# Kernel tuning notes

Hardware: AMD Instinct MI355X
Metric: run time of the kernel (lower is better)

Reference implementation:

```python
import jax, jax.numpy as jnp
import numpy as np

VOCAB = 4194304
EMBED = 128
BATCH = 16384
NUM_DENSE = 13
NUM_CAT = 26
BOT_DIMS = (512, 256, 128)
TOP_DIMS = (1024, 1024, 512, 256, 1)


def _dense_params(key, fan_in, fan_out):
    kw, kb = jax.random.split(key)
    w = jax.random.normal(kw, (fan_in, fan_out), jnp.float32) * np.sqrt(2.0 / (fan_in + fan_out))
    b = jax.random.normal(kb, (fan_out,), jnp.float32) * np.sqrt(1.0 / fan_out)
    return w, b


def setup_inputs() -> dict:
    key = jax.random.key(0)
    ks = jax.random.split(key, 16)
    inp = {}
    inp['x_dense'] = jax.random.normal(ks[0], (BATCH, NUM_DENSE), jnp.float32)
    inp['x_cat'] = jax.random.randint(ks[1], (BATCH, NUM_CAT), 0, VOCAB, dtype=jnp.int32)
    # embedding table: uniform(0,1) * 1/sqrt(vocab)
    inp['embedding_table'] = jax.random.uniform(ks[2], (VOCAB, EMBED), jnp.float32) * np.float32(1.0 / np.sqrt(VOCAB))
    # bottom MLP params
    fan_in = NUM_DENSE
    for i, d in enumerate(BOT_DIMS):
        w, b = _dense_params(ks[3 + i], fan_in, d)
        inp[f'w_bot{i}'], inp[f'b_bot{i}'] = w, b
        fan_in = d
    # top MLP params; input dim = embed_dim + n_triu(27) = 128 + 378 = 506
    n_feat = 1 + NUM_CAT  # 27
    fan_in = EMBED + n_feat * (n_feat + 1) // 2
    for i, d in enumerate(TOP_DIMS):
        w, b = _dense_params(ks[8 + i], fan_in, d)
        inp[f'w_top{i}'], inp[f'b_top{i}'] = w, b
        fan_in = d
    return inp


def _forward(x_dense, x_cat, embedding_table,
             w_bot0, b_bot0, w_bot1, b_bot1, w_bot2, b_bot2,
             w_top0, b_top0, w_top1, b_top1, w_top2, b_top2,
             w_top3, b_top3, w_top4, b_top4):
    B = x_dense.shape[0]
    # bottom MLP
    h = x_dense
    for w, b in ((w_bot0, b_bot0), (w_bot1, b_bot1), (w_bot2, b_bot2)):
        h = jax.nn.relu(h @ w + b)
    bot_out = h  # [B, 128]
    feat = bot_out.reshape(B, -1, EMBED)  # [B, 1, 128]
    # embedding gather (irregular access)
    idx = (x_cat.reshape(-1) % VOCAB)
    emb = embedding_table[idx].reshape(B, NUM_CAT, EMBED)  # [B, 26, 128]
    stack = jnp.concatenate([feat, emb], axis=1)  # [B, 27, 128]
    # self interaction + upper-triangular (incl. diagonal) extraction
    xact = jnp.einsum('bnd,bmd->bnm', stack, stack)  # [B, 27, 27]
    i, j = jnp.triu_indices(stack.shape[1])
    inter = xact[:, i, j]  # [B, 378]
    top = jnp.concatenate([bot_out, inter], axis=-1)  # [B, 506]
    tops = ((w_top0, b_top0), (w_top1, b_top1), (w_top2, b_top2), (w_top3, b_top3), (w_top4, b_top4))
    for li, (w, b) in enumerate(tops):
        top = top @ w + b
        if li < len(tops) - 1:
            top = jax.nn.relu(top)
    return top  # [B, 1] logits


def reference(x_dense, x_cat, embedding_table,
              w_bot0, b_bot0, w_bot1, b_bot1, w_bot2, b_bot2,
              w_top0, b_top0, w_top1, b_top1, w_top2, b_top2,
              w_top3, b_top3, w_top4, b_top4):
    return _forward(x_dense, x_cat, embedding_table,
                    w_bot0, b_bot0, w_bot1, b_bot1, w_bot2, b_bot2,
                    w_top0, b_top0, w_top1, b_top1, w_top2, b_top2,
                    w_top3, b_top3, w_top4, b_top4)
```

## Files before the change

### kernel.cpp

```cpp
#include <hip/hip_runtime.h>
#include <cstdint>
#include <cstddef>

#define BATCH 16384
#define VOCAB_MASK (4194304 - 1)

typedef __attribute__((ext_vector_type(4))) float f32x4;
typedef __attribute__((ext_vector_type(8))) __bf16 bf16x8;

static_assert(sizeof(bf16x8) == 16, "bf16x8 must be 16 bytes");

static __device__ __forceinline__ __bf16 f2bf(float f) {
  union { float f; unsigned u; } in; in.f = f;
  unsigned r = in.u + 0x7FFF + ((in.u >> 16) & 1);
  union { unsigned short s; __bf16 b; } out; out.s = (unsigned short)(r >> 16);
  return out.b;
}
static __device__ __forceinline__ float bf2f(__bf16 b) {
  union { __bf16 b; unsigned short s; } in; in.b = b;
  union { unsigned u; float f; } out; out.u = ((unsigned)in.s) << 16;
  return out.f;
}

#define GLDS16(g, l) __builtin_amdgcn_global_load_lds( \
    (const __attribute__((address_space(1))) unsigned int*)(g), \
    (__attribute__((address_space(3))) unsigned int*)(l), 16, 0, 0)

static __device__ __forceinline__ unsigned swz16(unsigned b) {
  return b ^ ((((b >> 6) & 3u) ^ ((b >> 8) & 3u)) << 4);
}
static __device__ __forceinline__ bf16x8 lds_frag(const char* smem, unsigned base,
                                                  unsigned r, unsigned cg) {
  unsigned b = r * 64u + cg;
  return *(const bf16x8*)(smem + base + swz16(b));
}

struct TJob { const float* W; __bf16* WT; int K, N, Kp, tx, off; };
struct TJobs { TJob j[7]; };

__global__ __launch_bounds__(256) void transpose_all(TJobs js, int njobs)
{
  __shared__ float tile[64][65];
  int b = blockIdx.x;
  int ji = 0;
  #pragma unroll
  for (int i = 1; i < 7; ++i) if (i < njobs && b >= js.j[i].off) ji = i;
  const TJob jb = js.j[ji];
  int lb = b - jb.off;
  int bx = lb % jb.tx, by = lb / jb.tx;
  const int kb = bx * 64, nb = by * 64;
  const int tx = threadIdx.x & 63, ty = threadIdx.x >> 6;
  #pragma unroll
  for (int i = 0; i < 64; i += 4) {
    int k = kb + ty + i, n = nb + tx;
    tile[ty + i][tx] = (k < jb.K && n < jb.N) ? jb.W[(size_t)k * jb.N + n] : 0.f;
  }
  __syncthreads();
  #pragma unroll
  for (int i = 0; i < 64; i += 4) {
    int n = nb + ty + i, k = kb + tx;
    if (n < jb.N && k < jb.Kp) jb.WT[(size_t)n * jb.Kp + k] = f2bf(tile[tx][ty + i]);
  }
}

__global__ __launch_bounds__(512, 2) void gemm_8ph(
    const __bf16* __restrict__ A, const __bf16* __restrict__ WT,
    const float* __restrict__ bias, __bf16* __restrict__ C,
    int N, int sA, int K, int gm)
{
  __shared__ __align__(16) char smem[65536];
  const int tid = threadIdx.x, lane = tid & 63, w = tid >> 6;
  const int wm = w >> 2, wn = w & 3;

  int nb = gridDim.x;
  int id = blockIdx.x;
  int swz = ((nb & 7) == 0) ? ((id & 7) * (nb >> 3) + (id >> 3)) : id;
  const int m0 = (swz % gm) * 256, n0 = (swz / gm) * 256;

  unsigned Ld[2]; const __bf16* sAp[2]; const __bf16* sBp[2];
  #pragma unroll
  for (int h = 0; h < 2; ++h) {
    unsigned L = h * 8192u + (unsigned)w * 1024u + (unsigned)lane * 16u;
    unsigned Ls = swz16(L);
    Ld[h] = L;
    int srow = Ls >> 6, scb = Ls & 63;
    sAp[h] = A  + (size_t)(m0 + srow) * sA + (scb >> 1);
    sBp[h] = WT + (size_t)(n0 + srow) * K  + (scb >> 1);
  }

  #define STAGE_A(kt, p) { GLDS16(sAp[0] + (kt)*32, smem + (p)*32768 + Ld[0]); \
                           GLDS16(sAp[1] + (kt)*32, smem + (p)*32768 + Ld[1]); }
  #define STAGE_B(kt, p) { GLDS16(sBp[0] + (kt)*32, smem + (p)*32768 + 16384 + Ld[0]); \
                           GLDS16(sBp[1] + (kt)*32, smem + (p)*32768 + 16384 + Ld[1]); }

  const unsigned cg = (lane >> 4) * 16u;
  const unsigned rA = (lane & 15);

  f32x4 acc[8][4] = {};
  const int KT = K >> 5;
  const int iters = KT >> 1;

  STAGE_B(0, 0); STAGE_A(0, 0); STAGE_B(1, 1);
  asm volatile("s_waitcnt vmcnt(2)" ::: "memory");
  __builtin_amdgcn_s_barrier();
  __builtin_amdgcn_sched_barrier(0);

  for (int i = 0; i < iters; ++i) {
    const int t = 2 * i;
    const bool more = (i + 1 < iters);

    bf16x8 a0[4], b0[4];
    #pragma unroll
    for (int m = 0; m < 4; ++m) a0[m] = lds_frag(smem, 0, wm * 128 + m * 16 + rA, cg);
    #pragma unroll
    for (int n = 0; n < 4; ++n) b0[n] = lds_frag(smem, 16384, wn * 64 + n * 16 + rA, cg);
    STAGE_A(t + 1, 1);
    __builtin_amdgcn_s_barrier();
    asm volatile("s_waitcnt lgkmcnt(0)" ::: "memory");
    __builtin_amdgcn_sched_barrier(0);
    __builtin_amdgcn_s_setprio(1);
    #pragma unroll
    for (int m = 0; m < 4; ++m)
      #pragma unroll
      for (int n = 0; n < 4; ++n)
        acc[m][n] = __builtin_amdgcn_mfma_f32_16x16x32_bf16(a0[m], b0[n], acc[m][n], 0, 0, 0);
    __builtin_amdgcn_s_setprio(0);
    __builtin_amdgcn_s_barrier();
    __builtin_amdgcn_sched_barrier(0);

    bf16x8 a1[4];
    #pragma unroll
    for (int m = 0; m < 4; ++m) a1[m] = lds_frag(smem, 0, wm * 128 + 64 + m * 16 + rA, cg);
    if (more) STAGE_B(t + 2, 0);
    __builtin_amdgcn_s_barrier();
    asm volatile("s_waitcnt lgkmcnt(0)" ::: "memory");
    __builtin_amdgcn_sched_barrier(0);
    __builtin_amdgcn_s_setprio(1);
    #pragma unroll
    for (int m = 0; m < 4; ++m)
      #pragma unroll
      for (int n = 0; n < 4; ++n)
        acc[4 + m][n] = __builtin_amdgcn_mfma_f32_16x16x32_bf16(a1[m], b0[n], acc[4 + m][n], 0, 0, 0);
    __builtin_amdgcn_s_setprio(0);
    if (more) { asm volatile("s_waitcnt vmcnt(2)" ::: "memory"); }
    else      { asm volatile("s_waitcnt vmcnt(0)" ::: "memory"); }
    __builtin_amdgcn_s_barrier();
    __builtin_amdgcn_sched_barrier(0);

    bf16x8 a2[4], b2[4];
    #pragma unroll
    for (int m = 0; m < 4; ++m) a2[m] = lds_frag(smem, 32768, wm * 128 + m * 16 + rA, cg);
    #pragma unroll
    for (int n = 0; n < 4; ++n) b2[n] = lds_frag(smem, 32768 + 16384, wn * 64 + n * 16 + rA, cg);
    if (more) STAGE_A(t + 2, 0);
    __builtin_amdgcn_s_barrier();
    asm volatile("s_waitcnt lgkmcnt(0)" ::: "memory");
    __builtin_amdgcn_sched_barrier(0);
    __builtin_amdgcn_s_setprio(1);
    #pragma unroll
    for (int m = 0; m < 4; ++m)
      #pragma unroll
      for (int n = 0; n < 4; ++n)
        acc[m][n] = __builtin_amdgcn_mfma_f32_16x16x32_bf16(a2[m], b2[n], acc[m][n], 0, 0, 0);
    __builtin_amdgcn_s_setprio(0);
    __builtin_amdgcn_s_barrier();
    __builtin_amdgcn_sched_barrier(0);

    bf16x8 a3[4];
    #pragma unroll
    for (int m = 0; m < 4; ++m) a3[m] = lds_frag(smem, 32768, wm * 128 + 64 + m * 16 + rA, cg);
    if (more) STAGE_B(t + 3, 1);
    __builtin_amdgcn_s_barrier();
    asm volatile("s_waitcnt lgkmcnt(0)" ::: "memory");
    __builtin_amdgcn_sched_barrier(0);
    __builtin_amdgcn_s_setprio(1);
    #pragma unroll
    for (int m = 0; m < 4; ++m)
      #pragma unroll
      for (int n = 0; n < 4; ++n)
        acc[4 + m][n] = __builtin_amdgcn_mfma_f32_16x16x32_bf16(a3[m], b2[n], acc[4 + m][n], 0, 0, 0);
    __builtin_amdgcn_s_setprio(0);
    if (more) { asm volatile("s_waitcnt vmcnt(2)" ::: "memory"); }
    __builtin_amdgcn_s_barrier();
    __builtin_amdgcn_sched_barrier(0);
  }

  #pragma unroll
  for (int n = 0; n < 4; ++n) {
    int col = n0 + wn * 64 + n * 16 + (lane & 15);
    float bv = bias[col];
    #pragma unroll
    for (int m = 0; m < 8; ++m) {
      #pragma unroll
      for (int r = 0; r < 4; ++r) {
        int row = m0 + wm * 128 + m * 16 + (lane >> 4) * 4 + r;
        float v = fmaxf(acc[m][n][r] + bv, 0.f);
        C[(size_t)row * N + col] = f2bf(v);
      }
    }
  }
  #undef STAGE_A
  #undef STAGE_B
}

__global__ __launch_bounds__(256) void gemm_glds(
    const __bf16* __restrict__ A, const __bf16* __restrict__ WT,
    const float* __restrict__ bias, __bf16* __restrict__ C,
    int N, int sA, int Kp)
{
  __shared__ __bf16 As[128][32];
  __shared__ __bf16 Bs[128][32];
  const int tid  = threadIdx.x;
  const int lane = tid & 63;
  const int wid  = tid >> 6;
  const int wr = wid >> 1, wc = wid & 1;
  const int m0 = blockIdx.x * 128, n0 = blockIdx.y * 128;

  const int srow = wid * 16 + (lane >> 2);
  const int scol = (lane & 3) * 8;
  const __bf16* Ag0 = A  + (size_t)(m0 + srow)      * sA + scol;
  const __bf16* Ag1 = A  + (size_t)(m0 + srow + 64) * sA + scol;
  const __bf16* Bg0 = WT + (size_t)(n0 + srow)      * Kp + scol;
  const __bf16* Bg1 = WT + (size_t)(n0 + srow + 64) * Kp + scol;
  __bf16* lA0 = &As[srow][scol];
  __bf16* lA1 = &As[srow + 64][scol];
  __bf16* lB0 = &Bs[srow][scol];
  __bf16* lB1 = &Bs[srow + 64][scol];

  f32x4 acc[4][4] = {};

  for (int k0 = 0; k0 < Kp; k0 += 32) {
    __syncthreads();
    GLDS16(Ag0 + k0, lA0);
    GLDS16(Ag1 + k0, lA1);
    GLDS16(Bg0 + k0, lB0);
    GLDS16(Bg1 + k0, lB1);
    __syncthreads();

    bf16x8 af[4], bfv[4];
    #pragma unroll
    for (int m = 0; m < 4; ++m)
      af[m] = *(const bf16x8*)&As[wr * 64 + m * 16 + (lane & 15)][(lane >> 4) * 8];
    #pragma unroll
    for (int n = 0; n < 4; ++n)
      bfv[n] = *(const bf16x8*)&Bs[wc * 64 + n * 16 + (lane & 15)][(lane >> 4) * 8];
    #pragma unroll
    for (int m = 0; m < 4; ++m)
      #pragma unroll
      for (int n = 0; n < 4; ++n)
        acc[m][n] = __builtin_amdgcn_mfma_f32_16x16x32_bf16(af[m], bfv[n], acc[m][n], 0, 0, 0);
  }

  #pragma unroll
  for (int m = 0; m < 4; ++m)
    #pragma unroll
    for (int n = 0; n < 4; ++n) {
      int col = n0 + wc * 64 + n * 16 + (lane & 15);
      float bv = bias[col];
      #pragma unroll
      for (int r = 0; r < 4; ++r) {
        int row = m0 + wr * 64 + m * 16 + (lane >> 4) * 4 + r;
        float v = fmaxf(acc[m][n][r] + bv, 0.f);
        C[(size_t)row * N + col] = f2bf(v);
      }
    }
}

__global__ __launch_bounds__(256) void gemm_f32a(
    const float* __restrict__ A, const __bf16* __restrict__ WT,
    const float* __restrict__ bias, __bf16* __restrict__ C,
    int N, int sA, int Kb, int Kp)
{
  __shared__ __bf16 As[128][40];
  __shared__ __bf16 Bs[128][40];
  const int tid  = threadIdx.x;
  const int lane = tid & 63;
  const int wid  = tid >> 6;
  const int wr = wid >> 1, wc = wid & 1;
  const int m0 = blockIdx.x * 128, n0 = blockIdx.y * 128;
  const int lrow = tid >> 2;
  const int lkk  = (tid & 3) * 8;

  f32x4 acc[4][4] = {};

  for (int k0 = 0; k0 < Kp; k0 += 32) {
    __syncthreads();
    #pragma unroll
    for (int it = 0; it < 2; ++it) {
      int row = lrow + it * 64;
      #pragma unroll
      for (int j = 0; j < 8; ++j) {
        int k = k0 + lkk + j;
        float v = (k < Kb) ? A[(size_t)(m0 + row) * sA + k] : 0.f;
        As[row][lkk + j] = f2bf(v);
      }
      *(bf16x8*)&Bs[row][lkk] = *(const bf16x8*)&WT[(size_t)(n0 + row) * Kp + k0 + lkk];
    }
    __syncthreads();

    bf16x8 af[4], bfv[4];
    #pragma unroll
    for (int m = 0; m < 4; ++m)
      af[m] = *(const bf16x8*)&As[wr * 64 + m * 16 + (lane & 15)][(lane >> 4) * 8];
    #pragma unroll
    for (int n = 0; n < 4; ++n)
      bfv[n] = *(const bf16x8*)&Bs[wc * 64 + n * 16 + (lane & 15)][(lane >> 4) * 8];
    #pragma unroll
    for (int m = 0; m < 4; ++m)
      #pragma unroll
      for (int n = 0; n < 4; ++n)
        acc[m][n] = __builtin_amdgcn_mfma_f32_16x16x32_bf16(af[m], bfv[n], acc[m][n], 0, 0, 0);
  }

  #pragma unroll
  for (int m = 0; m < 4; ++m)
    #pragma unroll
    for (int n = 0; n < 4; ++n) {
      int col = n0 + wc * 64 + n * 16 + (lane & 15);
      float bv = bias[col];
      #pragma unroll
      for (int r = 0; r < 4; ++r) {
        int row = m0 + wr * 64 + m * 16 + (lane >> 4) * 4 + r;
        float v = fmaxf(acc[m][n][r] + bv, 0.f);
        C[(size_t)row * N + col] = f2bf(v);
      }
    }
}

__global__ __launch_bounds__(256) void interact_mfma(
    const __bf16* __restrict__ bot, const int* __restrict__ xcat,
    const float* __restrict__ emb, __bf16* __restrict__ top_in)
{
  __shared__ __bf16 st[4][32][136];
  const int tid = threadIdx.x, lane = tid & 63, w = tid >> 6;
  const int s = blockIdx.x * 4 + w;

  {
    const __bf16* bp = bot + (size_t)s * 128 + lane * 2;
    st[w][0][lane * 2]     = bp[0];
    st[w][0][lane * 2 + 1] = bp[1];
  }
  const int* xr = xcat + (size_t)s * 26;
  #pragma unroll
  for (int r = 1; r < 27; ++r) {
    int ridx = xr[r - 1] & VOCAB_MASK;
    float2 v = *(const float2*)(emb + (size_t)ridx * 128 + lane * 2);
    st[w][r][lane * 2]     = f2bf(v.x);
    st[w][r][lane * 2 + 1] = f2bf(v.y);
  }
  #pragma unroll
  for (int r = 27; r < 32; ++r) {
    st[w][r][lane * 2]     = f2bf(0.f);
    st[w][r][lane * 2 + 1] = f2bf(0.f);
  }

  f32x4 a00 = {}, a01 = {}, a11 = {};
  #pragma unroll
  for (int k0 = 0; k0 < 4; ++k0) {
    bf16x8 fr0 = *(const bf16x8*)&st[w][(lane & 15)][k0 * 32 + (lane >> 4) * 8];
    bf16x8 fr1 = *(const bf16x8*)&st[w][16 + (lane & 15)][k0 * 32 + (lane >> 4) * 8];
    a00 = __builtin_amdgcn_mfma_f32_16x16x32_bf16(fr0, fr0, a00, 0, 0, 0);
    a01 = __builtin_amdgcn_mfma_f32_16x16x32_bf16(fr0, fr1, a01, 0, 0, 0);
    a11 = __builtin_amdgcn_mfma_f32_16x16x32_bf16(fr1, fr1, a11, 0, 0, 0);
  }

  __bf16* op = top_in + (size_t)s * 512;
  op[lane * 2]     = st[w][0][lane * 2];
  op[lane * 2 + 1] = st[w][0][lane * 2 + 1];
  if (lane < 6) op[506 + lane] = f2bf(0.f);

  const int jc = lane & 15, rb = (lane >> 4) * 4;
  #pragma unroll
  for (int r = 0; r < 4; ++r) {
    {
      int i = rb + r, j = jc;
      if (i <= j) op[128 + i * 27 - i * (i - 1) / 2 + (j - i)] = f2bf(a00[r]);
    }
    {
      int i = rb + r, j = 16 + jc;
      if (j <= 26) op[128 + i * 27 - i * (i - 1) / 2 + (j - i)] = f2bf(a01[r]);
    }
    {
      int i = 16 + rb + r, j = 16 + jc;
      if (i <= j && j <= 26) op[128 + i * 27 - i * (i - 1) / 2 + (j - i)] = f2bf(a11[r]);
    }
  }
}

__global__ __launch_bounds__(256) void final_kernel(
    const __bf16* __restrict__ t3, const float* __restrict__ w4,
    const float* __restrict__ b4, float* __restrict__ out)
{
  int row  = blockIdx.x * 4 + (threadIdx.x >> 6);
  int lane = threadIdx.x & 63;
  const __bf16* tr = &t3[(size_t)row * 256 + lane * 4];
  float acc = 0.f;
  #pragma unroll
  for (int j = 0; j < 4; ++j) acc += bf2f(tr[j]) * w4[lane * 4 + j];
  #pragma unroll
  for (int off = 32; off; off >>= 1) acc += __shfl_down(acc, off);
  if (lane == 0) out[row] = acc + b4[0];
}

extern "C" void kernel_launch(void* const* d_in, const int* in_sizes, int n_in,
                              void* d_out, int out_size, void* d_ws, size_t ws_size,
                              hipStream_t stream)
{
  const float* x_dense = (const float*)d_in[0];
  const int*   x_cat   = (const int*)d_in[1];
  const float* emb     = (const float*)d_in[2];
  const float* wb[3] = {(const float*)d_in[3], (const float*)d_in[5], (const float*)d_in[7]};
  const float* bb[3] = {(const float*)d_in[4], (const float*)d_in[6], (const float*)d_in[8]};
  const float* wt[5] = {(const float*)d_in[9],  (const float*)d_in[11], (const float*)d_in[13],
                        (const float*)d_in[15], (const float*)d_in[17]};
  const float* bt[5] = {(const float*)d_in[10], (const float*)d_in[12], (const float*)d_in[14],
                        (const float*)d_in[16], (const float*)d_in[18]};
  float* out = (float*)d_out;

  char* ws = (char*)d_ws;
  const size_t MB = 1ull << 20;
  __bf16* wt_b0 = (__bf16*)(ws + 0 * MB);
  __bf16* wt_b1 = (__bf16*)(ws + 1 * MB);
  __bf16* wt_b2 = (__bf16*)(ws + 2 * MB);
  __bf16* wt_t0 = (__bf16*)(ws + 3 * MB);
  __bf16* wt_t1 = (__bf16*)(ws + 4 * MB);
  __bf16* wt_t2 = (__bf16*)(ws + 6 * MB);
  __bf16* wt_t3 = (__bf16*)(ws + 7 * MB);
  __bf16* h2     = (__bf16*)(ws + 8 * MB);
  __bf16* top_in = (__bf16*)(ws + 12 * MB);
  __bf16* t2     = (__bf16*)(ws + 12 * MB);
  __bf16* h0     = (__bf16*)(ws + 28 * MB);
  __bf16* t1     = (__bf16*)(ws + 28 * MB);
  __bf16* t3     = (__bf16*)(ws + 28 * MB);
  __bf16* h1     = (__bf16*)(ws + 60 * MB);
  __bf16* t0     = (__bf16*)(ws + 60 * MB);

  TJobs js;
  const float* Ws[7] = {wb[0], wb[1], wb[2], wt[0], wt[1], wt[2], wt[3]};
  __bf16* WTs[7] = {wt_b0, wt_b1, wt_b2, wt_t0, wt_t1, wt_t2, wt_t3};
  int Ks[7]  = {13, 512, 256, 506, 1024, 1024, 512};
  int Ns[7]  = {512, 256, 128, 1024, 1024, 512, 256};
  int Kps[7] = {32, 512, 256, 512, 1024, 1024, 512};
  int off = 0;
  for (int i = 0; i < 7; ++i) {
    int tx = (Kps[i] + 63) / 64, ty = (Ns[i] + 63) / 64;
    js.j[i] = TJob{Ws[i], WTs[i], Ks[i], Ns[i], Kps[i], tx, off};
    off += tx * ty;
  }
  transpose_all<<<dim3(off), dim3(256), 0, stream>>>(js, 7);

  gemm_f32a<<<dim3(128, 4), dim3(256), 0, stream>>>(x_dense, wt_b0, bb[0], h0, 512, 13, 13, 32);
  gemm_glds<<<dim3(128, 2), dim3(256), 0, stream>>>(h0, wt_b1, bb[1], h1, 256, 512, 512);
  gemm_glds<<<dim3(128, 1), dim3(256), 0, stream>>>(h1, wt_b2, bb[2], h2, 128, 256, 256);

  interact_mfma<<<dim3(BATCH / 4), dim3(256), 0, stream>>>(h2, x_cat, emb, top_in);

  gemm_8ph<<<dim3(256), dim3(512), 0, stream>>>(top_in, wt_t0, bt[0], t0, 1024, 512, 512, 64);
  gemm_8ph<<<dim3(256), dim3(512), 0, stream>>>(t0, wt_t1, bt[1], t1, 1024, 1024, 1024, 64);
  gemm_glds<<<dim3(128, 4), dim3(256), 0, stream>>>(t1, wt_t2, bt[2], t2, 512, 1024, 1024);
  gemm_glds<<<dim3(128, 2), dim3(256), 0, stream>>>(t2, wt_t3, bt[3], t3, 256, 512, 512);

  final_kernel<<<dim3(BATCH / 4), dim3(256), 0, stream>>>(t3, wt[4], bt[4], out);
}
```

Baseline: 214.6 us.

## Fuse bottom MLP into one kernel and use pipelined 256x128 GEMM for top layer 2

The three bottom-MLP GEMM launches are merged into one kernel. Each 32-row block computes h0 and h1 in shared memory and writes only h2, which removes two launches and the global round trips of the h0/h1 intermediates. The third top-MLP layer (N=512) moves from the simple gemm_glds kernel to a new software-pipelined 256x128 tile variant of gemm_8ph, for better MFMA utilisation. The fused bottom kernel uses small 32-row tiles and reloads weight tiles in every block, which may limit its efficiency.

```diff
diff --git a/kernel.cpp b/kernel.cpp
--- a/kernel.cpp
+++ b/kernel.cpp
@@ -61,6 +61,130 @@
     int n = nb + ty + i, k = kb + tx;
     if (n < jb.N && k < jb.Kp) jb.WT[(size_t)n * jb.Kp + k] = f2bf(tile[tx][ty + i]);
   }
+}
+
+__global__ __launch_bounds__(256) void bottom_fused(
+    const float* __restrict__ x,
+    const __bf16* __restrict__ w0t, const float* __restrict__ b0,
+    const __bf16* __restrict__ w1t, const float* __restrict__ b1,
+    const __bf16* __restrict__ w2t, const float* __restrict__ b2,
+    __bf16* __restrict__ h2out)
+{
+  __shared__ __bf16 h0s[32][520];
+  __shared__ __bf16 h1s[32][264];
+  __shared__ __bf16 As[32][40];
+  __shared__ __bf16 Bs[256][32];
+  const int tid = threadIdx.x, lane = tid & 63, w = tid >> 6;
+  const int r0 = blockIdx.x * 32;
+  const int srow_b = lane >> 2;
+  const int scol_b = (lane & 3) * 8;
+  const unsigned rA = lane & 15, cgw = (lane >> 4) * 8;
+
+  for (int idx = tid; idx < 32 * 40; idx += 256) {
+    int row = idx / 40, k = idx - row * 40;
+    float v = (k < 13) ? x[(size_t)(r0 + row) * 13 + k] : 0.f;
+    As[row][k] = f2bf(v);
+  }
+
+  #pragma unroll
+  for (int p = 0; p < 2; ++p) {
+    __syncthreads();
+    #pragma unroll
+    for (int c = 0; c < 4; ++c) {
+      int row = w * 64 + c * 16 + srow_b;
+      GLDS16(w0t + (size_t)(p * 256 + row) * 32 + scol_b, &Bs[row][scol_b]);
+    }
+    __syncthreads();
+    bf16x8 a[2], bv[4];
+    #pragma unroll
+    for (int m = 0; m < 2; ++m) a[m] = *(const bf16x8*)&As[rA + m * 16][cgw];
+    #pragma unroll
+    for (int n = 0; n < 4; ++n) bv[n] = *(const bf16x8*)&Bs[w * 64 + n * 16 + rA][cgw];
+    f32x4 acc[2][4] = {};
+    #pragma unroll
+    for (int m = 0; m < 2; ++m)
+      #pragma unroll
+      for (int n = 0; n < 4; ++n)
+        acc[m][n] = __builtin_amdgcn_mfma_f32_16x16x32_bf16(a[m], bv[n], acc[m][n], 0, 0, 0);
+    #pragma unroll
+    for (int m = 0; m < 2; ++m)
+      #pragma unroll
+      for (int n = 0; n < 4; ++n) {
+        int col = p * 256 + w * 64 + n * 16 + (int)rA;
+        float bb = b0[col];
+        #pragma unroll
+        for (int r = 0; r < 4; ++r) {
+          int row = m * 16 + (lane >> 4) * 4 + r;
+          h0s[row][col] = f2bf(fmaxf(acc[m][n][r] + bb, 0.f));
+        }
+      }
+  }
+
+  f32x4 acc1[2][4] = {};
+  for (int k0 = 0; k0 < 512; k0 += 32) {
+    __syncthreads();
+    #pragma unroll
+    for (int c = 0; c < 4; ++c) {
+      int row = w * 64 + c * 16 + srow_b;
+      GLDS16(w1t + (size_t)row * 512 + k0 + scol_b, &Bs[row][scol_b]);
+    }
+    __syncthreads();
+    bf16x8 a[2], bv[4];
+    #pragma unroll
+    for (int m = 0; m < 2; ++m) a[m] = *(const bf16x8*)&h0s[rA + m * 16][k0 + cgw];
+    #pragma unroll
+    for (int n = 0; n < 4; ++n) bv[n] = *(const bf16x8*)&Bs[w * 64 + n * 16 + rA][cgw];
+    #pragma unroll
+    for (int m = 0; m < 2; ++m)
+      #pragma unroll
+      for (int n = 0; n < 4; ++n)
+        acc1[m][n] = __builtin_amdgcn_mfma_f32_16x16x32_bf16(a[m], bv[n], acc1[m][n], 0, 0, 0);
+  }
+  #pragma unroll
+  for (int m = 0; m < 2; ++m)
+    #pragma unroll
+    for (int n = 0; n < 4; ++n) {
+      int col = w * 64 + n * 16 + (int)rA;
+      float bb = b1[col];
+      #pragma unroll
+      for (int r = 0; r < 4; ++r) {
+        int row = m * 16 + (lane >> 4) * 4 + r;
+        h1s[row][col] = f2bf(fmaxf(acc1[m][n][r] + bb, 0.f));
+      }
+    }
+
+  f32x4 acc2[2][2] = {};
+  for (int k0 = 0; k0 < 256; k0 += 32) {
+    __syncthreads();
+    #pragma unroll
+    for (int c = 0; c < 2; ++c) {
+      int row = w * 32 + c * 16 + srow_b;
+      GLDS16(w2t + (size_t)row * 256 + k0 + scol_b, &Bs[row][scol_b]);
+    }
+    __syncthreads();
+    bf16x8 a[2], bv[2];
+    #pragma unroll
+    for (int m = 0; m < 2; ++m) a[m] = *(const bf16x8*)&h1s[rA + m * 16][k0 + cgw];
+    #pragma unroll
+    for (int n = 0; n < 2; ++n) bv[n] = *(const bf16x8*)&Bs[w * 32 + n * 16 + rA][cgw];
+    #pragma unroll
+    for (int m = 0; m < 2; ++m)
+      #pragma unroll
+      for (int n = 0; n < 2; ++n)
+        acc2[m][n] = __builtin_amdgcn_mfma_f32_16x16x32_bf16(a[m], bv[n], acc2[m][n], 0, 0, 0);
+  }
+  #pragma unroll
+  for (int m = 0; m < 2; ++m)
+    #pragma unroll
+    for (int n = 0; n < 2; ++n) {
+      int col = w * 32 + n * 16 + (int)rA;
+      float bb = b2[col];
+      #pragma unroll
+      for (int r = 0; r < 4; ++r) {
+        int row = m * 16 + (lane >> 4) * 4 + r;
+        h2out[(size_t)(r0 + row) * 128 + col] = f2bf(fmaxf(acc2[m][n][r] + bb, 0.f));
+      }
+    }
 }
 
 __global__ __launch_bounds__(512, 2) void gemm_8ph(
@@ -97,8 +221,7 @@
   const unsigned rA = (lane & 15);
 
   f32x4 acc[8][4] = {};
-  const int KT = K >> 5;
-  const int iters = KT >> 1;
+  const int iters = (K >> 5) >> 1;
 
   STAGE_B(0, 0); STAGE_A(0, 0); STAGE_B(1, 1);
   asm volatile("s_waitcnt vmcnt(2)" ::: "memory");
@@ -201,6 +324,149 @@
   }
   #undef STAGE_A
   #undef STAGE_B
+}
+
+__global__ __launch_bounds__(512, 2) void gemm_8ph_n128(
+    const __bf16* __restrict__ A, const __bf16* __restrict__ WT,
+    const float* __restrict__ bias, __bf16* __restrict__ C,
+    int N, int sA, int K, int gm)
+{
+  __shared__ __align__(16) char smem[49152];
+  const int tid = threadIdx.x, lane = tid & 63, w = tid >> 6;
+  const int wm = w >> 1, wn = w & 1;
+
+  int nb = gridDim.x;
+  int id = blockIdx.x;
+  int swz = ((nb & 7) == 0) ? ((id & 7) * (nb >> 3) + (id >> 3)) : id;
+  const int m0 = (swz % gm) * 256, n0 = (swz / gm) * 128;
+
+  unsigned Ld[2]; const __bf16* sAp[2]; const __bf16* sBp0;
+  #pragma unroll
+  for (int h = 0; h < 2; ++h) {
+    unsigned L = h * 8192u + (unsigned)w * 1024u + (unsigned)lane * 16u;
+    unsigned Ls = swz16(L);
+    Ld[h] = L;
+    int srow = Ls >> 6, scb = Ls & 63;
+    sAp[h] = A + (size_t)(m0 + srow) * sA + (scb >> 1);
+  }
+  {
+    unsigned L = (unsigned)w * 1024u + (unsigned)lane * 16u;
+    unsigned Ls = swz16(L);
+    int srow = Ls >> 6, scb = Ls & 63;
+    sBp0 = WT + (size_t)(n0 + srow) * K + (scb >> 1);
+  }
+
+  #define STAGE_A2(kt, p) { GLDS16(sAp[0] + (kt)*32, smem + (p)*24576 + Ld[0]); \
+                            GLDS16(sAp[1] + (kt)*32, smem + (p)*24576 + Ld[1]); }
+  #define STAGE_B1(kt, p) { GLDS16(sBp0 + (kt)*32, smem + (p)*24576 + 16384 + Ld[0]); }
+
+  const unsigned cg = (lane >> 4) * 16u;
+  const unsigned rA = (lane & 15);
+
+  f32x4 acc[4][4] = {};
+  const int iters = (K >> 5) >> 1;
+
+  STAGE_B1(0, 0); STAGE_A2(0, 0); STAGE_B1(1, 1);
+  asm volatile("s_waitcnt vmcnt(1)" ::: "memory");
+  __builtin_amdgcn_s_barrier();
+  __builtin_amdgcn_sched_barrier(0);
+
+  for (int i = 0; i < iters; ++i) {
+    const int t = 2 * i;
+    const bool more = (i + 1 < iters);
+
+    bf16x8 a0[2], b0[4];
+    #pragma unroll
+    for (int m = 0; m < 2; ++m) a0[m] = lds_frag(smem, 0, wm * 64 + m * 16 + rA, cg);
+    #pragma unroll
+    for (int n = 0; n < 4; ++n) b0[n] = lds_frag(smem, 16384, wn * 64 + n * 16 + rA, cg);
+    STAGE_A2(t + 1, 1);
+    __builtin_amdgcn_s_barrier();
+    asm volatile("s_waitcnt lgkmcnt(0)" ::: "memory");
+    __builtin_amdgcn_sched_barrier(0);
+    __builtin_amdgcn_s_setprio(1);
+    #pragma unroll
+    for (int m = 0; m < 2; ++m)
+      #pragma unroll
+      for (int n = 0; n < 4; ++n)
+        acc[m][n] = __builtin_amdgcn_mfma_f32_16x16x32_bf16(a0[m], b0[n], acc[m][n], 0, 0, 0);
+    __builtin_amdgcn_s_setprio(0);
+    __builtin_amdgcn_s_barrier();
+    __builtin_amdgcn_sched_barrier(0);
+
+    bf16x8 a1[2];
+    #pragma unroll
+    for (int m = 0; m < 2; ++m) a1[m] = lds_frag(smem, 0, wm * 64 + 32 + m * 16 + rA, cg);
+    if (more) STAGE_B1(t + 2, 0);
+    __builtin_amdgcn_s_barrier();
+    asm volatile("s_waitcnt lgkmcnt(0)" ::: "memory");
+    __builtin_amdgcn_sched_barrier(0);
+    __builtin_amdgcn_s_setprio(1);
+    #pragma unroll
+    for (int m = 0; m < 2; ++m)
+      #pragma unroll
+      for (int n = 0; n < 4; ++n)
+        acc[2 + m][n] = __builtin_amdgcn_mfma_f32_16x16x32_bf16(a1[m], b0[n], acc[2 + m][n], 0, 0, 0);
+    __builtin_amdgcn_s_setprio(0);
+    if (more) { asm volatile("s_waitcnt vmcnt(1)" ::: "memory"); }
+    else      { asm volatile("s_waitcnt vmcnt(0)" ::: "memory"); }
+    __builtin_amdgcn_s_barrier();
+    __builtin_amdgcn_sched_barrier(0);
+
+    bf16x8 a2[2], b2[4];
+    #pragma unroll
+    for (int m = 0; m < 2; ++m) a2[m] = lds_frag(smem, 24576, wm * 64 + m * 16 + rA, cg);
+    #pragma unroll
+    for (int n = 0; n < 4; ++n) b2[n] = lds_frag(smem, 24576 + 16384, wn * 64 + n * 16 + rA, cg);
+    if (more) STAGE_A2(t + 2, 0);
+    __builtin_amdgcn_s_barrier();
+    asm volatile("s_waitcnt lgkmcnt(0)" ::: "memory");
+    __builtin_amdgcn_sched_barrier(0);
+    __builtin_amdgcn_s_setprio(1);
+    #pragma unroll
+    for (int m = 0; m < 2; ++m)
+      #pragma unroll
+      for (int n = 0; n < 4; ++n)
+        acc[m][n] = __builtin_amdgcn_mfma_f32_16x16x32_bf16(a2[m], b2[n], acc[m][n], 0, 0, 0);
+    __builtin_amdgcn_s_setprio(0);
+    __builtin_amdgcn_s_barrier();
+    __builtin_amdgcn_sched_barrier(0);
+
+    bf16x8 a3[2];
+    #pragma unroll
+    for (int m = 0; m < 2; ++m) a3[m] = lds_frag(smem, 24576, wm * 64 + 32 + m * 16 + rA, cg);
+    if (more) STAGE_B1(t + 3, 1);
+    __builtin_amdgcn_s_barrier();
+    asm volatile("s_waitcnt lgkmcnt(0)" ::: "memory");
+    __builtin_amdgcn_sched_barrier(0);
+    __builtin_amdgcn_s_setprio(1);
+    #pragma unroll
+    for (int m = 0; m < 2; ++m)
+      #pragma unroll
+      for (int n = 0; n < 4; ++n)
+        acc[2 + m][n] = __builtin_amdgcn_mfma_f32_16x16x32_bf16(a3[m], b2[n], acc[2 + m][n], 0, 0, 0);
+    __builtin_amdgcn_s_setprio(0);
+    if (more) { asm volatile("s_waitcnt vmcnt(1)" ::: "memory"); }
+    __builtin_amdgcn_s_barrier();
+    __builtin_amdgcn_sched_barrier(0);
+  }
+
+  #pragma unroll
+  for (int n = 0; n < 4; ++n) {
+    int col = n0 + wn * 64 + n * 16 + (lane & 15);
+    float bv = bias[col];
+    #pragma unroll
+    for (int m = 0; m < 4; ++m) {
+      #pragma unroll
+      for (int r = 0; r < 4; ++r) {
+        int row = m0 + wm * 64 + m * 16 + (lane >> 4) * 4 + r;
+        float v = fmaxf(acc[m][n][r] + bv, 0.f);
+        C[(size_t)row * N + col] = f2bf(v);
+      }
+    }
+  }
+  #undef STAGE_A2
+  #undef STAGE_B1
 }
 
 __global__ __launch_bounds__(256) void gemm_glds(
@@ -235,67 +501,6 @@
     GLDS16(Ag1 + k0, lA1);
     GLDS16(Bg0 + k0, lB0);
     GLDS16(Bg1 + k0, lB1);
-    __syncthreads();
-
-    bf16x8 af[4], bfv[4];
-    #pragma unroll
-    for (int m = 0; m < 4; ++m)
-      af[m] = *(const bf16x8*)&As[wr * 64 + m * 16 + (lane & 15)][(lane >> 4) * 8];
-    #pragma unroll
-    for (int n = 0; n < 4; ++n)
-      bfv[n] = *(const bf16x8*)&Bs[wc * 64 + n * 16 + (lane & 15)][(lane >> 4) * 8];
-    #pragma unroll
-    for (int m = 0; m < 4; ++m)
-      #pragma unroll
-      for (int n = 0; n < 4; ++n)
-        acc[m][n] = __builtin_amdgcn_mfma_f32_16x16x32_bf16(af[m], bfv[n], acc[m][n], 0, 0, 0);
-  }
-
-  #pragma unroll
-  for (int m = 0; m < 4; ++m)
-    #pragma unroll
-    for (int n = 0; n < 4; ++n) {
-      int col = n0 + wc * 64 + n * 16 + (lane & 15);
-      float bv = bias[col];
-      #pragma unroll
-      for (int r = 0; r < 4; ++r) {
-        int row = m0 + wr * 64 + m * 16 + (lane >> 4) * 4 + r;
-        float v = fmaxf(acc[m][n][r] + bv, 0.f);
-        C[(size_t)row * N + col] = f2bf(v);
-      }
-    }
-}
-
-__global__ __launch_bounds__(256) void gemm_f32a(
-    const float* __restrict__ A, const __bf16* __restrict__ WT,
-    const float* __restrict__ bias, __bf16* __restrict__ C,
-    int N, int sA, int Kb, int Kp)
-{
-  __shared__ __bf16 As[128][40];
-  __shared__ __bf16 Bs[128][40];
-  const int tid  = threadIdx.x;
-  const int lane = tid & 63;
-  const int wid  = tid >> 6;
-  const int wr = wid >> 1, wc = wid & 1;
-  const int m0 = blockIdx.x * 128, n0 = blockIdx.y * 128;
-  const int lrow = tid >> 2;
-  const int lkk  = (tid & 3) * 8;
-
-  f32x4 acc[4][4] = {};
-
-  for (int k0 = 0; k0 < Kp; k0 += 32) {
-    __syncthreads();
-    #pragma unroll
-    for (int it = 0; it < 2; ++it) {
-      int row = lrow + it * 64;
-      #pragma unroll
-      for (int j = 0; j < 8; ++j) {
-        int k = k0 + lkk + j;
-        float v = (k < Kb) ? A[(size_t)(m0 + row) * sA + k] : 0.f;
-        As[row][lkk + j] = f2bf(v);
-      }
-      *(bf16x8*)&Bs[row][lkk] = *(const bf16x8*)&WT[(size_t)(n0 + row) * Kp + k0 + lkk];
-    }
     __syncthreads();
 
     bf16x8 af[4], bfv[4];
@@ -429,10 +634,8 @@
   __bf16* h2     = (__bf16*)(ws + 8 * MB);
   __bf16* top_in = (__bf16*)(ws + 12 * MB);
   __bf16* t2     = (__bf16*)(ws + 12 * MB);
-  __bf16* h0     = (__bf16*)(ws + 28 * MB);
   __bf16* t1     = (__bf16*)(ws + 28 * MB);
   __bf16* t3     = (__bf16*)(ws + 28 * MB);
-  __bf16* h1     = (__bf16*)(ws + 60 * MB);
   __bf16* t0     = (__bf16*)(ws + 60 * MB);
 
   TJobs js;
@@ -449,15 +652,14 @@
   }
   transpose_all<<<dim3(off), dim3(256), 0, stream>>>(js, 7);
 
-  gemm_f32a<<<dim3(128, 4), dim3(256), 0, stream>>>(x_dense, wt_b0, bb[0], h0, 512, 13, 13, 32);
-  gemm_glds<<<dim3(128, 2), dim3(256), 0, stream>>>(h0, wt_b1, bb[1], h1, 256, 512, 512);
-  gemm_glds<<<dim3(128, 1), dim3(256), 0, stream>>>(h1, wt_b2, bb[2], h2, 128, 256, 256);
+  bottom_fused<<<dim3(BATCH / 32), dim3(256), 0, stream>>>(
+      x_dense, wt_b0, bb[0], wt_b1, bb[1], wt_b2, bb[2], h2);
 
   interact_mfma<<<dim3(BATCH / 4), dim3(256), 0, stream>>>(h2, x_cat, emb, top_in);
 
   gemm_8ph<<<dim3(256), dim3(512), 0, stream>>>(top_in, wt_t0, bt[0], t0, 1024, 512, 512, 64);
   gemm_8ph<<<dim3(256), dim3(512), 0, stream>>>(t0, wt_t1, bt[1], t1, 1024, 1024, 1024, 64);
-  gemm_glds<<<dim3(128, 4), dim3(256), 0, stream>>>(t1, wt_t2, bt[2], t2, 512, 1024, 1024);
+  gemm_8ph_n128<<<dim3(256), dim3(512), 0, stream>>>(t1, wt_t2, bt[2], t2, 512, 1024, 1024, 64);
   gemm_glds<<<dim3(128, 2), dim3(256), 0, stream>>>(t2, wt_t3, bt[3], t3, 256, 512, 512);
 
   final_kernel<<<dim3(BATCH / 4), dim3(256), 0, stream>>>(t3, wt[4], bt[4], out);
```

New measurement: 198.8 us. 7.4% less time.
